# Kernel tuning notes

Hardware: AMD Instinct MI355X
Metric: run time of the kernel (lower is better)

## Reference

```python
import jax, jax.numpy as jnp
import numpy as np

N = 262144      # number of octants at the finest depth (in_h == out_h for stride=1)
C_IN = 32
C_OUT = 64
K3 = 27         # 3**3 filter taps


def setup_inputs() -> dict:
    key = jax.random.key(0)
    k1, k2, k3, k4 = jax.random.split(key, 4)
    inputsignal = jax.random.normal(k1, (N, C_IN), dtype=jnp.float32)
    weights = jax.random.normal(k2, (K3, C_IN, C_OUT), dtype=jnp.float32)
    # Octree neighbor table: indices into the N octants; -1 marks missing
    neigh = jax.random.randint(k3, (N, K3), 0, N, dtype=jnp.int32)
    invalid = jax.random.uniform(k4, (N, K3)) < 0.15
    neigh = jnp.where(invalid, jnp.int32(-1), neigh)
    return {"inputsignal": inputsignal, "weights": weights, "neigh": neigh}


def reference(inputsignal, weights, neigh):
    # Gather neighbor features; invalid (-1) neighbors contribute zeros,
    # matching buffer.fill_(0); buffer[valid] = inputsignal[neigh_i[valid]].
    valid = neigh >= 0                                   # [N, K3]
    safe_idx = jnp.where(valid, neigh, 0)                # clamp for gather
    gathered = inputsignal[safe_idx]                     # [N, K3, C_in]
    gathered = jnp.where(valid[..., None], gathered, 0.0)
    # Filter-wise GEMM: out[n, o] = sum_{k,c} gathered[n,k,c] * W[k,c,o]
    # (equivalent to mm(buffer.flatten(1,2), weights.flatten(0,1)))
    out = jnp.einsum("nkc,kco->no", gathered, weights)   # [N, C_out]
    return out
```

## Files before the change

### kernel.cpp

```cpp
#include <hip/hip_runtime.h>
#include <hip/hip_bf16.h>


typedef float f32x4 __attribute__((ext_vector_type(4)));
typedef __bf16 bf16x8 __attribute__((ext_vector_type(8)));

#define NN 262144
#define CI 32
#define CO 64
#define KK 27
#define WPAD 40
#define THREADS 1024
#define OCT_PER_BLOCK 256

__device__ __forceinline__ ushort f2bf_rne(float f) {
  union { float f; unsigned u; } v; v.f = f;
  unsigned u = v.u;
  u += 0x7FFFu + ((u >> 16) & 1u);
  return (ushort)(u >> 16);
}

__global__ __launch_bounds__(THREADS, 1) void octconv_kernel(
    const float* __restrict__ input,
    const float* __restrict__ weights,
    const int*   __restrict__ neigh,
    float*       __restrict__ out)
{
  __shared__ ushort w_lds[KK * CO * WPAD];

  const int tid = threadIdx.x;

  for (int i = tid; i < KK * CI * CO; i += THREADS) {
    const int k   = i >> 11;
    const int rem = i & 2047;
    const int c   = rem >> 6;
    const int o   = rem & 63;
    w_lds[(k * CO + o) * WPAD + c] = f2bf_rne(weights[i]);
  }
  __syncthreads();

  const int wave = tid >> 6;
  const int lane = tid & 63;
  const int g    = lane >> 4;
  const int r16  = lane & 15;
  const int oct_base = blockIdx.x * OCT_PER_BLOCK + wave * 16;
  const int row = oct_base + r16;

  int nb[KK];
  const int* __restrict__ nrow = neigh + row * KK;
#pragma unroll
  for (int k = 0; k < KK; ++k) nb[k] = nrow[k];

  f32x4 acc0 = {0.f, 0.f, 0.f, 0.f};
  f32x4 acc1 = acc0, acc2 = acc0, acc3 = acc0;

#pragma unroll
  for (int k = 0; k < KK; ++k) {
    const int  idx   = nb[k];
    const bool valid = idx >= 0;
    const float* __restrict__ p =
        input + (size_t)(valid ? idx : 0) * CI + g * 8;
    f32x4 v0 = *(const f32x4*)p;
    f32x4 v1 = *(const f32x4*)(p + 4);
    if (!valid) {
      v0 = (f32x4){0.f, 0.f, 0.f, 0.f};
      v1 = (f32x4){0.f, 0.f, 0.f, 0.f};
    }
    bf16x8 a;
    a[0] = (__bf16)v0[0]; a[1] = (__bf16)v0[1];
    a[2] = (__bf16)v0[2]; a[3] = (__bf16)v0[3];
    a[4] = (__bf16)v1[0]; a[5] = (__bf16)v1[1];
    a[6] = (__bf16)v1[2]; a[7] = (__bf16)v1[3];

    const ushort* wk = &w_lds[(k * CO + r16) * WPAD + g * 8];
    bf16x8 b0 = *(const bf16x8*)(wk + 0 * 16 * WPAD);
    bf16x8 b1 = *(const bf16x8*)(wk + 1 * 16 * WPAD);
    bf16x8 b2 = *(const bf16x8*)(wk + 2 * 16 * WPAD);
    bf16x8 b3 = *(const bf16x8*)(wk + 3 * 16 * WPAD);

    acc0 = __builtin_amdgcn_mfma_f32_16x16x32_bf16(a, b0, acc0, 0, 0, 0);
    acc1 = __builtin_amdgcn_mfma_f32_16x16x32_bf16(a, b1, acc1, 0, 0, 0);
    acc2 = __builtin_amdgcn_mfma_f32_16x16x32_bf16(a, b2, acc2, 0, 0, 0);
    acc3 = __builtin_amdgcn_mfma_f32_16x16x32_bf16(a, b3, acc3, 0, 0, 0);
  }

  float* __restrict__ obase = out + (size_t)(oct_base + g * 4) * CO + r16;
#pragma unroll
  for (int rr = 0; rr < 4; ++rr) {
    obase[rr * CO +  0] = acc0[rr];
    obase[rr * CO + 16] = acc1[rr];
    obase[rr * CO + 32] = acc2[rr];
    obase[rr * CO + 48] = acc3[rr];
  }
}

extern "C" void kernel_launch(void* const* d_in, const int* in_sizes, int n_in,
                              void* d_out, int out_size, void* d_ws, size_t ws_size,
                              hipStream_t stream) {
  const float* input   = (const float*)d_in[0];
  const float* weights = (const float*)d_in[1];
  const int*   neigh   = (const int*)d_in[2];
  float*       out     = (float*)d_out;

  dim3 grid(NN / OCT_PER_BLOCK);
  octconv_kernel<<<grid, THREADS, 0, stream>>>(input, weights, neigh, out);
}
```

Baseline: 139.7 us.

## Pre-convert input to bf16 in workspace and tile four octant groups per wave

Adds a pre-pass kernel that converts the fp32 input features to bf16 in the workspace, so each neighbor gather reads 16 bytes instead of 32 and needs no per-element conversion. Each wave now handles four 16-octant tiles per filter tap, reusing the LDS weight fragments across them, and the grid shrinks accordingly. Neighbor indices are read on the fly instead of preloaded. The extra conversion launch adds traffic and launch overhead, the larger per-thread accumulator set raises register pressure, and fewer blocks may reduce parallelism across the GPU.

```diff
diff --git a/kernel.cpp b/kernel.cpp
--- a/kernel.cpp
+++ b/kernel.cpp
@@ -2,8 +2,10 @@
 #include <hip/hip_bf16.h>
 
 
-typedef float f32x4 __attribute__((ext_vector_type(4)));
+typedef float  f32x4  __attribute__((ext_vector_type(4)));
 typedef __bf16 bf16x8 __attribute__((ext_vector_type(8)));
+typedef int    i32x4  __attribute__((ext_vector_type(4)));
+typedef ushort u16x4  __attribute__((ext_vector_type(4)));
 
 #define NN 262144
 #define CI 32
@@ -11,7 +13,9 @@
 #define KK 27
 #define WPAD 40
 #define THREADS 1024
-#define OCT_PER_BLOCK 256
+#define TILE_T 4
+#define OCT_PER_WAVE (16 * TILE_T)
+#define OCT_PER_BLOCK (OCT_PER_WAVE * 16)
 
 __device__ __forceinline__ ushort f2bf_rne(float f) {
   union { float f; unsigned u; } v; v.f = f;
@@ -20,8 +24,19 @@
   return (ushort)(u >> 16);
 }
 
-__global__ __launch_bounds__(THREADS, 1) void octconv_kernel(
-    const float* __restrict__ input,
+__global__ __launch_bounds__(256) void cvt_input_kernel(
+    const float* __restrict__ in, ushort* __restrict__ out) {
+  const int i = (blockIdx.x * 256 + threadIdx.x) * 4;
+  f32x4 v = *(const f32x4*)(in + i);
+  u16x4 o;
+  o[0] = f2bf_rne(v[0]); o[1] = f2bf_rne(v[1]);
+  o[2] = f2bf_rne(v[2]); o[3] = f2bf_rne(v[3]);
+  *(u16x4*)(out + i) = o;
+}
+
+template <bool BF16IN>
+__global__ __launch_bounds__(THREADS, 4) void octconv_kernel(
+    const void* __restrict__ input_v,
     const float* __restrict__ weights,
     const int*   __restrict__ neigh,
     float*       __restrict__ out)
@@ -29,7 +44,6 @@
   __shared__ ushort w_lds[KK * CO * WPAD];
 
   const int tid = threadIdx.x;
-
   for (int i = tid; i < KK * CI * CO; i += THREADS) {
     const int k   = i >> 11;
     const int rem = i & 2047;
@@ -43,54 +57,67 @@
   const int lane = tid & 63;
   const int g    = lane >> 4;
   const int r16  = lane & 15;
-  const int oct_base = blockIdx.x * OCT_PER_BLOCK + wave * 16;
-  const int row = oct_base + r16;
+  const int oct_base = blockIdx.x * OCT_PER_BLOCK + wave * OCT_PER_WAVE;
 
-  int nb[KK];
-  const int* __restrict__ nrow = neigh + row * KK;
+  const int* __restrict__ nptr[TILE_T];
 #pragma unroll
-  for (int k = 0; k < KK; ++k) nb[k] = nrow[k];
+  for (int t = 0; t < TILE_T; ++t)
+    nptr[t] = neigh + (size_t)(oct_base + t * 16 + r16) * KK;
 
-  f32x4 acc0 = {0.f, 0.f, 0.f, 0.f};
-  f32x4 acc1 = acc0, acc2 = acc0, acc3 = acc0;
+  f32x4 acc[TILE_T][4];
+#pragma unroll
+  for (int t = 0; t < TILE_T; ++t)
+#pragma unroll
+    for (int b = 0; b < 4; ++b)
+      acc[t][b] = (f32x4){0.f, 0.f, 0.f, 0.f};
 
 #pragma unroll
   for (int k = 0; k < KK; ++k) {
-    const int  idx   = nb[k];
-    const bool valid = idx >= 0;
-    const float* __restrict__ p =
-        input + (size_t)(valid ? idx : 0) * CI + g * 8;
-    f32x4 v0 = *(const f32x4*)p;
-    f32x4 v1 = *(const f32x4*)(p + 4);
-    if (!valid) {
-      v0 = (f32x4){0.f, 0.f, 0.f, 0.f};
-      v1 = (f32x4){0.f, 0.f, 0.f, 0.f};
+    bf16x8 bf[4];
+#pragma unroll
+    for (int b = 0; b < 4; ++b)
+      bf[b] = *(const bf16x8*)&w_lds[(k * CO + r16 + 16 * b) * WPAD + g * 8];
+
+#pragma unroll
+    for (int t = 0; t < TILE_T; ++t) {
+      const int idx = nptr[t][k];
+      bf16x8 a;
+      if (BF16IN) {
+        const ushort* __restrict__ ip =
+            (const ushort*)input_v + (size_t)(idx < 0 ? 0 : idx) * CI + g * 8;
+        i32x4 u = *(const i32x4*)ip;
+        if (idx < 0) u = (i32x4){0, 0, 0, 0};
+        a = __builtin_bit_cast(bf16x8, u);
+      } else {
+        const float* __restrict__ ip =
+            (const float*)input_v + (size_t)(idx < 0 ? 0 : idx) * CI + g * 8;
+        f32x4 v0 = *(const f32x4*)ip;
+        f32x4 v1 = *(const f32x4*)(ip + 4);
+        if (idx < 0) {
+          v0 = (f32x4){0.f, 0.f, 0.f, 0.f};
+          v1 = (f32x4){0.f, 0.f, 0.f, 0.f};
+        }
+        a[0] = (__bf16)v0[0]; a[1] = (__bf16)v0[1];
+        a[2] = (__bf16)v0[2]; a[3] = (__bf16)v0[3];
+        a[4] = (__bf16)v1[0]; a[5] = (__bf16)v1[1];
+        a[6] = (__bf16)v1[2]; a[7] = (__bf16)v1[3];
+      }
+#pragma unroll
+      for (int b = 0; b < 4; ++b)
+        acc[t][b] = __builtin_amdgcn_mfma_f32_16x16x32_bf16(a, bf[b], acc[t][b], 0, 0, 0);
     }
-    bf16x8 a;
-    a[0] = (__bf16)v0[0]; a[1] = (__bf16)v0[1];
-    a[2] = (__bf16)v0[2]; a[3] = (__bf16)v0[3];
-    a[4] = (__bf16)v1[0]; a[5] = (__bf16)v1[1];
-    a[6] = (__bf16)v1[2]; a[7] = (__bf16)v1[3];
-
-    const ushort* wk = &w_lds[(k * CO + r16) * WPAD + g * 8];
-    bf16x8 b0 = *(const bf16x8*)(wk + 0 * 16 * WPAD);
-    bf16x8 b1 = *(const bf16x8*)(wk + 1 * 16 * WPAD);
-    bf16x8 b2 = *(const bf16x8*)(wk + 2 * 16 * WPAD);
-    bf16x8 b3 = *(const bf16x8*)(wk + 3 * 16 * WPAD);
-
-    acc0 = __builtin_amdgcn_mfma_f32_16x16x32_bf16(a, b0, acc0, 0, 0, 0);
-    acc1 = __builtin_amdgcn_mfma_f32_16x16x32_bf16(a, b1, acc1, 0, 0, 0);
-    acc2 = __builtin_amdgcn_mfma_f32_16x16x32_bf16(a, b2, acc2, 0, 0, 0);
-    acc3 = __builtin_amdgcn_mfma_f32_16x16x32_bf16(a, b3, acc3, 0, 0, 0);
   }
 
-  float* __restrict__ obase = out + (size_t)(oct_base + g * 4) * CO + r16;
 #pragma unroll
-  for (int rr = 0; rr < 4; ++rr) {
-    obase[rr * CO +  0] = acc0[rr];
-    obase[rr * CO + 16] = acc1[rr];
-    obase[rr * CO + 32] = acc2[rr];
-    obase[rr * CO + 48] = acc3[rr];
+  for (int t = 0; t < TILE_T; ++t) {
+    float* __restrict__ obase =
+        out + (size_t)(oct_base + t * 16 + g * 4) * CO + r16;
+#pragma unroll
+    for (int rr = 0; rr < 4; ++rr) {
+#pragma unroll
+      for (int b = 0; b < 4; ++b)
+        obase[rr * CO + 16 * b] = acc[t][b][rr];
+    }
   }
 }
 
@@ -102,6 +129,16 @@
   const int*   neigh   = (const int*)d_in[2];
   float*       out     = (float*)d_out;
 
+  const size_t bf16_bytes = (size_t)NN * CI * sizeof(ushort);
+  const bool use_bf16 = ws_size >= bf16_bytes;
+
   dim3 grid(NN / OCT_PER_BLOCK);
-  octconv_kernel<<<grid, THREADS, 0, stream>>>(input, weights, neigh, out);
+
+  if (use_bf16) {
+    ushort* in_bf16 = (ushort*)d_ws;
+    cvt_input_kernel<<<dim3((NN * CI) / (256 * 4)), 256, 0, stream>>>(input, in_bf16);
+    octconv_kernel<true><<<grid, THREADS, 0, stream>>>(in_bf16, weights, neigh, out);
+  } else {
+    octconv_kernel<false><<<grid, THREADS, 0, stream>>>(input, weights, neigh, out);
+  }
 }
```

Result: slower. 156.8 us (+12.3%).
